# Kernel optimization log

Hardware: AMD Instinct MI355X
Metric: run time of the kernel (lower is better)

## Reference

```python
import jax, jax.numpy as jnp
import numpy as np

EPS = 1e-6          # RMSNorm eps
SINK_EPS = 1e-12    # Sinkhorn denominator eps
N_ITER = 5          # sinkhorn_iters


def setup_inputs() -> dict:
    key = jax.random.key(0)
    ks = jax.random.split(key, 12)
    B, T, H, D = 2, 2048, 4, 2048
    FD = H * D
    W_SCALE = 0.02  # keep gate logits in a non-saturated sigmoid range
    return {
        "x": jax.random.normal(ks[0], (B, T, H, D), jnp.float32),
        "norm_w": jnp.ones((FD,), jnp.float32),
        "w_pre": jax.random.normal(ks[1], (H, FD), jnp.float32) * W_SCALE,
        "w_res": jax.random.normal(ks[2], (H * H, FD), jnp.float32) * W_SCALE,
        "w_post": jax.random.normal(ks[3], (H, FD), jnp.float32) * W_SCALE,
        "alpha_pre": jax.random.uniform(ks[4], (1,), jnp.float32),
        "alpha_res": jax.random.uniform(ks[5], (1,), jnp.float32),
        "alpha_post": jax.random.uniform(ks[6], (1,), jnp.float32),
        "s_pre": jax.random.normal(ks[7], (H,), jnp.float32),
        "s_res": jax.random.normal(ks[8], (H, H), jnp.float32),
        "s_post": jax.random.normal(ks[9], (H,), jnp.float32),
        "w_inner": jax.random.normal(ks[10], (D, D), jnp.float32) * (1.0 / np.sqrt(D)),
    }


def sinkhorn_knopp(logits, n_iter):
    # Doubly-stochastic projection over last two dims.
    m = jnp.exp(logits - jnp.max(logits, axis=(-2, -1), keepdims=True))
    for _ in range(n_iter):
        m = m / (jnp.sum(m, axis=-1, keepdims=True) + SINK_EPS)
        m = m / (jnp.sum(m, axis=-2, keepdims=True) + SINK_EPS)
    return m


def reference(x, norm_w, w_pre, w_res, w_post, alpha_pre, alpha_res, alpha_post,
              s_pre, s_res, s_post, w_inner):
    b, t, h, d = x.shape
    flat = x.reshape(b, t, h * d)
    # RMSNorm over flat dim
    var = jnp.mean(flat * flat, axis=-1, keepdims=True)
    normed = norm_w * flat * jax.lax.rsqrt(var + EPS)
    # Gate projections (Linear, no bias => x @ W.T)
    a_raw = alpha_pre * (normed @ w_pre.T) + s_pre                     # (b,t,h)
    b_raw = (alpha_res * (normed @ w_res.T)).reshape(b, t, h, h) + s_res
    c_raw = alpha_post * (normed @ w_post.T) + s_post                  # (b,t,h)
    a_l = jax.nn.sigmoid(a_raw)
    c_l = 2.0 * jax.nn.sigmoid(c_raw)
    b_l = sinkhorn_knopp(b_raw, N_ITER)
    # split: inner input
    inner_in = jnp.einsum('bth,bthd->btd', a_l, x)
    # inner layer: bias-free linear
    inner_out = inner_in @ w_inner.T
    # combine
    carry = jnp.einsum('bthk,btkd->bthd', b_l, x)
    write = jnp.einsum('bth,btd->bthd', c_l, inner_out)
    return carry + write
```

## Files before the change

kernel.cpp:

```cpp
#include <hip/hip_runtime.h>
#include <hip/hip_bf16.h>

#define FD 8192
#define DD 2048
#define NH 4
#define NT 4096
#define NG 24
#define NGP 32
#define KSPLIT 32
#define KC (FD / KSPLIT)
#define CH 64

typedef __attribute__((ext_vector_type(4))) float f32x4;
typedef __attribute__((ext_vector_type(8))) short short8;

__device__ inline unsigned short f2bf(float f) {
  __hip_bfloat16 h = __float2bfloat16(f);
  unsigned short u; __builtin_memcpy(&u, &h, 2); return u;
}
__device__ inline float bf2f(unsigned short u) {
  __hip_bfloat16 h; __builtin_memcpy(&h, &u, 2); return __bfloat162float(h);
}

__global__ __launch_bounds__(256) void k_prep(
    const float* __restrict__ w_inner,
    const float* __restrict__ w_pre,
    const float* __restrict__ w_res,
    const float* __restrict__ w_post,
    const float* __restrict__ norm_w,
    unsigned short* __restrict__ w_inner_bf,
    unsigned short* __restrict__ wnb)
{
  int stride = gridDim.x * blockDim.x;
  int gid = blockIdx.x * blockDim.x + threadIdx.x;
  for (int i = gid; i < DD * DD; i += stride) w_inner_bf[i] = f2bf(w_inner[i]);
  for (int i = gid; i < NGP * FD; i += stride) {
    int j = i >> 13, k = i & (FD - 1);
    float w = (j < 4) ? w_pre[j * FD + k]
            : (j < 20) ? w_res[(j - 4) * FD + k]
            : (j < 24) ? w_post[(j - 20) * FD + k]
            : 0.0f;
    wnb[i] = f2bf(w * norm_w[k]);
  }
}

__global__ __launch_bounds__(256) void k_gates(
    const float* __restrict__ x, const unsigned short* __restrict__ wnb,
    float* __restrict__ partial ,
    unsigned short* __restrict__ xb )
{
  __shared__ unsigned short xs[128][72];
  const int tb = blockIdx.x;
  const int ks = blockIdx.y;
  const int tid = threadIdx.x;
  const int wave = tid >> 6, lane = tid & 63;
  const int lr = lane & 15, kg = lane >> 4;
  const int t0 = tb * 128;
  const int k0 = ks * KC;
  const int sr = tid >> 4;
  const int sc = (tid & 15) * 4;

  float ssq[8];
#pragma unroll
  for (int i = 0; i < 8; ++i) ssq[i] = 0.f;
  f32x4 acc[2][2] = {};

  for (int ch = 0; ch < KC; ch += CH) {
    __syncthreads();
#pragma unroll
    for (int it = 0; it < 8; ++it) {
      int r = it * 16 + sr;
      size_t goff = (size_t)(t0 + r) * FD + k0 + ch + sc;
      f32x4 v = *(const f32x4*)&x[goff];
      ssq[it] += v.x * v.x + v.y * v.y + v.z * v.z + v.w * v.w;
      ushort4 o;
      o.x = f2bf(v.x); o.y = f2bf(v.y); o.z = f2bf(v.z); o.w = f2bf(v.w);
      *(ushort4*)&xs[r][sc] = o;
      *(ushort4*)&xb[goff] = o;
    }
    __syncthreads();
#pragma unroll
    for (int kk = 0; kk < CH; kk += 32) {
      short8 a[2], b[2];
#pragma unroll
      for (int m = 0; m < 2; ++m)
        a[m] = *(const short8*)&xs[wave * 32 + m * 16 + lr][kk + kg * 8];
#pragma unroll
      for (int n = 0; n < 2; ++n)
        b[n] = *(const short8*)&wnb[(size_t)(n * 16 + lr) * FD + k0 + ch + kk + kg * 8];
#pragma unroll
      for (int m = 0; m < 2; ++m)
#pragma unroll
        for (int n = 0; n < 2; ++n)
          acc[m][n] = __builtin_amdgcn_mfma_f32_16x16x32_bf16(a[m], b[n], acc[m][n], 0, 0, 0);
    }
  }

  float* base = &partial[(size_t)ks * NT * (NG + 1)];
#pragma unroll
  for (int m = 0; m < 2; ++m)
#pragma unroll
    for (int n = 0; n < 2; ++n) {
      int g = n * 16 + lr;
      if (g < NG) {
#pragma unroll
        for (int r = 0; r < 4; ++r) {
          int row = wave * 32 + m * 16 + kg * 4 + r;
          base[(size_t)(t0 + row) * (NG + 1) + g] = acc[m][n][r];
        }
      }
    }
#pragma unroll
  for (int it = 0; it < 8; ++it) {
    float v = ssq[it];
    v += __shfl_xor(v, 1);
    v += __shfl_xor(v, 2);
    v += __shfl_xor(v, 4);
    v += __shfl_xor(v, 8);
    if ((tid & 15) == 0) {
      int row = it * 16 + sr;
      base[(size_t)(t0 + row) * (NG + 1) + NG] = v;
    }
  }
}

__global__ __launch_bounds__(256) void k_scalars(
    const float* __restrict__ partial,
    const float* __restrict__ alpha_pre, const float* __restrict__ alpha_res,
    const float* __restrict__ alpha_post,
    const float* __restrict__ s_pre, const float* __restrict__ s_res,
    const float* __restrict__ s_post,
    float* __restrict__ gates )
{
  int t = blockIdx.x * blockDim.x + threadIdx.x;
  if (t >= NT) return;
  float acc[NG + 1];
#pragma unroll
  for (int j = 0; j <= NG; ++j) acc[j] = 0.f;
  for (int s = 0; s < KSPLIT; ++s) {
    const float* p = &partial[((size_t)s * NT + t) * (NG + 1)];
#pragma unroll
    for (int j = 0; j <= NG; ++j) acc[j] += p[j];
  }
  float rinv = rsqrtf(acc[NG] * (1.0f / FD) + 1e-6f);
  float ap = alpha_pre[0], ar = alpha_res[0], apo = alpha_post[0];

  float out[NG];
#pragma unroll
  for (int h = 0; h < 4; ++h)
    out[h] = 1.f / (1.f + expf(-(ap * rinv * acc[h] + s_pre[h])));
#pragma unroll
  for (int h = 0; h < 4; ++h)
    out[4 + h] = 2.f / (1.f + expf(-(apo * rinv * acc[20 + h] + s_post[h])));

  float m[16]; float mx = -1e30f;
#pragma unroll
  for (int j = 0; j < 16; ++j) {
    float br = ar * rinv * acc[4 + j] + s_res[j];
    m[j] = br; mx = fmaxf(mx, br);
  }
#pragma unroll
  for (int j = 0; j < 16; ++j) m[j] = expf(m[j] - mx);
#pragma unroll
  for (int it = 0; it < 5; ++it) {
#pragma unroll
    for (int h = 0; h < 4; ++h) {
      float rs = m[h*4] + m[h*4+1] + m[h*4+2] + m[h*4+3];
      float inv = 1.f / (rs + 1e-12f);
      m[h*4] *= inv; m[h*4+1] *= inv; m[h*4+2] *= inv; m[h*4+3] *= inv;
    }
#pragma unroll
    for (int k = 0; k < 4; ++k) {
      float cs = m[k] + m[4+k] + m[8+k] + m[12+k];
      float inv = 1.f / (cs + 1e-12f);
      m[k] *= inv; m[4+k] *= inv; m[8+k] *= inv; m[12+k] *= inv;
    }
  }
#pragma unroll
  for (int j = 0; j < 16; ++j) out[8 + j] = m[j];

  float* gt = &gates[(size_t)t * 24];
#pragma unroll
  for (int j = 0; j < NG; ++j) gt[j] = out[j];
}

__global__ __launch_bounds__(256) void k_inner_in(
    const unsigned short* __restrict__ xb, const float* __restrict__ gates,
    unsigned short* __restrict__ inner_in)
{
  int t = blockIdx.x, tid = threadIdx.x;
  const float* g = &gates[(size_t)t * 24];
  float a0 = g[0], a1 = g[1], a2 = g[2], a3 = g[3];
  const unsigned short* xt = &xb[(size_t)t * FD];
  int d = tid * 8;
  short8 h0 = *(const short8*)&xt[0 * DD + d];
  short8 h1 = *(const short8*)&xt[1 * DD + d];
  short8 h2 = *(const short8*)&xt[2 * DD + d];
  short8 h3 = *(const short8*)&xt[3 * DD + d];
  short8 o;
#pragma unroll
  for (int j = 0; j < 8; ++j) {
    float s = a0 * bf2f((unsigned short)h0[j]) + a1 * bf2f((unsigned short)h1[j])
            + a2 * bf2f((unsigned short)h2[j]) + a3 * bf2f((unsigned short)h3[j]);
    o[j] = (short)f2bf(s);
  }
  *(short8*)&inner_in[(size_t)t * DD + d] = o;
}

__global__ __launch_bounds__(256) void k_gemm(
    const unsigned short* __restrict__ A,
    const unsigned short* __restrict__ B,
    unsigned short* __restrict__ C)
{
  __shared__ unsigned short As[128 * 64];
  __shared__ unsigned short Bs[128 * 64];
  const int bid = blockIdx.x;
  const int bm = bid >> 4, bn = bid & 15;
  const int tid = threadIdx.x;
  const int wave = tid >> 6, lane = tid & 63;
  const int wm = wave >> 1, wn_ = wave & 1;
  const int lr = lane & 15, kg = lane >> 4;

  const int srow = tid >> 3;
  const int scol = (tid & 7) * 8;
  const unsigned short* a_src = &A[(size_t)(bm * 128 + srow) * 2048 + scol];
  const unsigned short* b_src = &B[(size_t)(bn * 128 + srow) * 2048 + scol];

  f32x4 acc[4][4] = {};

  for (int kt = 0; kt < 2048; kt += 64) {
    __syncthreads();
#pragma unroll
    for (int it = 0; it < 4; ++it)
      __builtin_amdgcn_global_load_lds(
          (const __attribute__((address_space(1))) void*)(a_src + (size_t)it * 32 * 2048 + kt),
          (__attribute__((address_space(3))) void*)(&As[it * 2048 + tid * 8]), 16, 0, 0);
#pragma unroll
    for (int it = 0; it < 4; ++it)
      __builtin_amdgcn_global_load_lds(
          (const __attribute__((address_space(1))) void*)(b_src + (size_t)it * 32 * 2048 + kt),
          (__attribute__((address_space(3))) void*)(&Bs[it * 2048 + tid * 8]), 16, 0, 0);
    __syncthreads();
#pragma unroll
    for (int kk = 0; kk < 64; kk += 32) {
      short8 a[4], b[4];
#pragma unroll
      for (int m = 0; m < 4; ++m)
        a[m] = *(const short8*)&As[(wm * 64 + m * 16 + lr) * 64 + kk + kg * 8];
#pragma unroll
      for (int n = 0; n < 4; ++n)
        b[n] = *(const short8*)&Bs[(wn_ * 64 + n * 16 + lr) * 64 + kk + kg * 8];
#pragma unroll
      for (int m = 0; m < 4; ++m)
#pragma unroll
        for (int n = 0; n < 4; ++n)
          acc[m][n] = __builtin_amdgcn_mfma_f32_16x16x32_bf16(a[m], b[n], acc[m][n], 0, 0, 0);
    }
  }

  const int row_base = bm * 128 + wm * 64;
  const int col_base = bn * 128 + wn_ * 64;
#pragma unroll
  for (int m = 0; m < 4; ++m)
#pragma unroll
    for (int n = 0; n < 4; ++n) {
      int col = col_base + n * 16 + lr;
#pragma unroll
      for (int r = 0; r < 4; ++r) {
        int row = row_base + m * 16 + kg * 4 + r;
        C[(size_t)row * 2048 + col] = f2bf(acc[m][n][r]);
      }
    }
}

__global__ __launch_bounds__(256) void k_out(
    const unsigned short* __restrict__ xb, const float* __restrict__ gates,
    const unsigned short* __restrict__ inner_out, float* __restrict__ out)
{
  int t = blockIdx.x, tid = threadIdx.x;
  const float* g = &gates[(size_t)t * 24];
  float c[4], bl[16];
#pragma unroll
  for (int h = 0; h < 4; ++h) c[h] = g[4 + h];
#pragma unroll
  for (int j = 0; j < 16; ++j) bl[j] = g[8 + j];
  const unsigned short* xt = &xb[(size_t)t * FD];
  float* ot = &out[(size_t)t * FD];
  int d = tid * 8;
  short8 xh[4];
#pragma unroll
  for (int h = 0; h < 4; ++h) xh[h] = *(const short8*)&xt[h * DD + d];
  short8 iu = *(const short8*)&inner_out[(size_t)t * DD + d];
  float io[8], xf[4][8];
#pragma unroll
  for (int j = 0; j < 8; ++j) io[j] = bf2f((unsigned short)iu[j]);
#pragma unroll
  for (int h = 0; h < 4; ++h)
#pragma unroll
    for (int j = 0; j < 8; ++j) xf[h][j] = bf2f((unsigned short)xh[h][j]);
#pragma unroll
  for (int h = 0; h < 4; ++h) {
    f32x4 o0, o1;
#pragma unroll
    for (int j = 0; j < 4; ++j) {
      o0[j] = c[h] * io[j]     + bl[h*4+0] * xf[0][j]     + bl[h*4+1] * xf[1][j]
                               + bl[h*4+2] * xf[2][j]     + bl[h*4+3] * xf[3][j];
      o1[j] = c[h] * io[j + 4] + bl[h*4+0] * xf[0][j + 4] + bl[h*4+1] * xf[1][j + 4]
                               + bl[h*4+2] * xf[2][j + 4] + bl[h*4+3] * xf[3][j + 4];
    }
    *(f32x4*)&ot[h * DD + d] = o0;
    *(f32x4*)&ot[h * DD + d + 4] = o1;
  }
}

extern "C" void kernel_launch(void* const* d_in, const int* in_sizes, int n_in,
                              void* d_out, int out_size, void* d_ws, size_t ws_size,
                              hipStream_t stream) {
  const float* x          = (const float*)d_in[0];
  const float* norm_w     = (const float*)d_in[1];
  const float* w_pre      = (const float*)d_in[2];
  const float* w_res      = (const float*)d_in[3];
  const float* w_post     = (const float*)d_in[4];
  const float* alpha_pre  = (const float*)d_in[5];
  const float* alpha_res  = (const float*)d_in[6];
  const float* alpha_post = (const float*)d_in[7];
  const float* s_pre      = (const float*)d_in[8];
  const float* s_res      = (const float*)d_in[9];
  const float* s_post     = (const float*)d_in[10];
  const float* w_inner    = (const float*)d_in[11];
  float* out = (float*)d_out;

  char* ws = (char*)d_ws;
  size_t off = 0;
  auto alloc = [&](size_t bytes) -> void* {
    void* p = ws + off;
    off = (off + bytes + 255) & ~(size_t)255;
    return p;
  };
  unsigned short* w_inner_bf = (unsigned short*)alloc((size_t)DD * DD * 2);
  unsigned short* inner_in   = (unsigned short*)alloc((size_t)NT * DD * 2);
  unsigned short* inner_out  = (unsigned short*)alloc((size_t)NT * DD * 2);
  unsigned short* wnb        = (unsigned short*)alloc((size_t)NGP * FD * 2);
  unsigned short* xb         = (unsigned short*)alloc((size_t)NT * FD * 2);
  float* partial = (float*)alloc((size_t)KSPLIT * NT * (NG + 1) * 4);
  float* gates   = (float*)alloc((size_t)NT * 24 * 4);

  k_prep<<<1024, 256, 0, stream>>>(w_inner, w_pre, w_res, w_post, norm_w, w_inner_bf, wnb);
  k_gates<<<dim3(32, 32), 256, 0, stream>>>(x, wnb, partial, xb);
  k_scalars<<<16, 256, 0, stream>>>(partial, alpha_pre, alpha_res, alpha_post,
                                    s_pre, s_res, s_post, gates);
  k_inner_in<<<4096, 256, 0, stream>>>(xb, gates, inner_in);
  k_gemm<<<512, 256, 0, stream>>>(inner_in, w_inner_bf, inner_out);
  k_out<<<4096, 256, 0, stream>>>(xb, gates, inner_out, out);
}
```

Before: 175.1 us.

## Move x bf16 conversion and sum-of-squares into prep; load gate tiles via LDS DMA

The fp32-to-bf16 conversion of x and the per-token sum of squares move into k_prep, one block per token, with extra blocks that convert the weights using vector loads. k_gates then reads the bf16 x through global_load_lds straight into a 64KB LDS tile and runs the MFMA loop without re-staging. The goal is a simpler, more memory-efficient gate GEMM and a smaller partial buffer. In exchange, the bf16 x is now written and then read back by a separate kernel, and the large LDS allocation limits occupancy in k_gates.

```diff
diff --git a/kernel.cpp b/kernel.cpp
--- a/kernel.cpp
+++ b/kernel.cpp
@@ -9,7 +9,6 @@
 #define NGP 32
 #define KSPLIT 32
 #define KC (FD / KSPLIT)
-#define CH 64
 
 typedef __attribute__((ext_vector_type(4))) float f32x4;
 typedef __attribute__((ext_vector_type(8))) short short8;
@@ -23,33 +22,64 @@
 }
 
 __global__ __launch_bounds__(256) void k_prep(
+    const float* __restrict__ x,
     const float* __restrict__ w_inner,
     const float* __restrict__ w_pre,
     const float* __restrict__ w_res,
     const float* __restrict__ w_post,
     const float* __restrict__ norm_w,
+    unsigned short* __restrict__ xb,
+    float* __restrict__ ssq_out,
     unsigned short* __restrict__ w_inner_bf,
     unsigned short* __restrict__ wnb)
 {
-  int stride = gridDim.x * blockDim.x;
-  int gid = blockIdx.x * blockDim.x + threadIdx.x;
-  for (int i = gid; i < DD * DD; i += stride) w_inner_bf[i] = f2bf(w_inner[i]);
-  for (int i = gid; i < NGP * FD; i += stride) {
-    int j = i >> 13, k = i & (FD - 1);
-    float w = (j < 4) ? w_pre[j * FD + k]
-            : (j < 20) ? w_res[(j - 4) * FD + k]
-            : (j < 24) ? w_post[(j - 20) * FD + k]
-            : 0.0f;
-    wnb[i] = f2bf(w * norm_w[k]);
+  const int tid = threadIdx.x;
+  if (blockIdx.x < NT) {
+    const int t = blockIdx.x;
+    const float* xt = &x[(size_t)t * FD];
+    unsigned short* xo = &xb[(size_t)t * FD];
+    float ss = 0.f;
+#pragma unroll
+    for (int it = 0; it < 8; ++it) {
+      int d = (it * 256 + tid) * 4;
+      f32x4 v = *(const f32x4*)&xt[d];
+      ss += v.x * v.x + v.y * v.y + v.z * v.z + v.w * v.w;
+      ushort4 o;
+      o.x = f2bf(v.x); o.y = f2bf(v.y); o.z = f2bf(v.z); o.w = f2bf(v.w);
+      *(ushort4*)&xo[d] = o;
+    }
+#pragma unroll
+    for (int off = 1; off < 64; off <<= 1) ss += __shfl_xor(ss, off);
+    __shared__ float red[4];
+    if ((tid & 63) == 0) red[tid >> 6] = ss;
+    __syncthreads();
+    if (tid == 0) ssq_out[t] = red[0] + red[1] + red[2] + red[3];
+  } else {
+    const int wid = (blockIdx.x - NT) * 256 + tid;
+#pragma unroll
+    for (int it = 0; it < 4; ++it) {
+      int i = wid * 16 + it * 4;
+      f32x4 v = *(const f32x4*)&w_inner[i];
+      ushort4 o;
+      o.x = f2bf(v.x); o.y = f2bf(v.y); o.z = f2bf(v.z); o.w = f2bf(v.w);
+      *(ushort4*)&w_inner_bf[i] = o;
+    }
+    {
+      int j = wid >> 13, k = wid & (FD - 1);
+      float w = (j < 4) ? w_pre[j * FD + k]
+              : (j < 20) ? w_res[(j - 4) * FD + k]
+              : (j < 24) ? w_post[(j - 20) * FD + k]
+              : 0.0f;
+      wnb[wid] = f2bf(w * norm_w[k]);
+    }
   }
 }
 
 __global__ __launch_bounds__(256) void k_gates(
-    const float* __restrict__ x, const unsigned short* __restrict__ wnb,
-    float* __restrict__ partial ,
-    unsigned short* __restrict__ xb )
-{
-  __shared__ unsigned short xs[128][72];
+    const unsigned short* __restrict__ xb, const unsigned short* __restrict__ wnb,
+    float* __restrict__ partial )
+{
+  __shared__ unsigned short As[128 * 256];
   const int tb = blockIdx.x;
   const int ks = blockIdx.y;
   const int tid = threadIdx.x;
@@ -57,46 +87,33 @@
   const int lr = lane & 15, kg = lane >> 4;
   const int t0 = tb * 128;
   const int k0 = ks * KC;
-  const int sr = tid >> 4;
-  const int sc = (tid & 15) * 4;
-
-  float ssq[8];
-#pragma unroll
-  for (int i = 0; i < 8; ++i) ssq[i] = 0.f;
+
+  const unsigned short* src = &xb[(size_t)(t0 + (tid >> 5)) * FD + k0 + (tid & 31) * 8];
+#pragma unroll
+  for (int it = 0; it < 16; ++it)
+    __builtin_amdgcn_global_load_lds(
+        (const __attribute__((address_space(1))) void*)(src + (size_t)(it * 8) * FD),
+        (__attribute__((address_space(3))) void*)(&As[it * 2048 + tid * 8]), 16, 0, 0);
+  __syncthreads();
+
   f32x4 acc[2][2] = {};
-
-  for (int ch = 0; ch < KC; ch += CH) {
-    __syncthreads();
-#pragma unroll
-    for (int it = 0; it < 8; ++it) {
-      int r = it * 16 + sr;
-      size_t goff = (size_t)(t0 + r) * FD + k0 + ch + sc;
-      f32x4 v = *(const f32x4*)&x[goff];
-      ssq[it] += v.x * v.x + v.y * v.y + v.z * v.z + v.w * v.w;
-      ushort4 o;
-      o.x = f2bf(v.x); o.y = f2bf(v.y); o.z = f2bf(v.z); o.w = f2bf(v.w);
-      *(ushort4*)&xs[r][sc] = o;
-      *(ushort4*)&xb[goff] = o;
-    }
-    __syncthreads();
-#pragma unroll
-    for (int kk = 0; kk < CH; kk += 32) {
-      short8 a[2], b[2];
-#pragma unroll
-      for (int m = 0; m < 2; ++m)
-        a[m] = *(const short8*)&xs[wave * 32 + m * 16 + lr][kk + kg * 8];
+#pragma unroll
+  for (int kk = 0; kk < KC; kk += 32) {
+    short8 a[2], b[2];
+#pragma unroll
+    for (int m = 0; m < 2; ++m)
+      a[m] = *(const short8*)&As[(wave * 32 + m * 16 + lr) * 256 + kk + kg * 8];
+#pragma unroll
+    for (int n = 0; n < 2; ++n)
+      b[n] = *(const short8*)&wnb[(size_t)(n * 16 + lr) * FD + k0 + kk + kg * 8];
+#pragma unroll
+    for (int m = 0; m < 2; ++m)
 #pragma unroll
       for (int n = 0; n < 2; ++n)
-        b[n] = *(const short8*)&wnb[(size_t)(n * 16 + lr) * FD + k0 + ch + kk + kg * 8];
-#pragma unroll
-      for (int m = 0; m < 2; ++m)
-#pragma unroll
-        for (int n = 0; n < 2; ++n)
-          acc[m][n] = __builtin_amdgcn_mfma_f32_16x16x32_bf16(a[m], b[n], acc[m][n], 0, 0, 0);
-    }
-  }
-
-  float* base = &partial[(size_t)ks * NT * (NG + 1)];
+        acc[m][n] = __builtin_amdgcn_mfma_f32_16x16x32_bf16(a[m], b[n], acc[m][n], 0, 0, 0);
+  }
+
+  float* base = &partial[(size_t)ks * NT * NG];
 #pragma unroll
   for (int m = 0; m < 2; ++m)
 #pragma unroll
@@ -106,26 +123,14 @@
 #pragma unroll
         for (int r = 0; r < 4; ++r) {
           int row = wave * 32 + m * 16 + kg * 4 + r;
-          base[(size_t)(t0 + row) * (NG + 1) + g] = acc[m][n][r];
+          base[(size_t)(t0 + row) * NG + g] = acc[m][n][r];
         }
       }
     }
-#pragma unroll
-  for (int it = 0; it < 8; ++it) {
-    float v = ssq[it];
-    v += __shfl_xor(v, 1);
-    v += __shfl_xor(v, 2);
-    v += __shfl_xor(v, 4);
-    v += __shfl_xor(v, 8);
-    if ((tid & 15) == 0) {
-      int row = it * 16 + sr;
-      base[(size_t)(t0 + row) * (NG + 1) + NG] = v;
-    }
-  }
 }
 
 __global__ __launch_bounds__(256) void k_scalars(
-    const float* __restrict__ partial,
+    const float* __restrict__ partial, const float* __restrict__ ssq,
     const float* __restrict__ alpha_pre, const float* __restrict__ alpha_res,
     const float* __restrict__ alpha_post,
     const float* __restrict__ s_pre, const float* __restrict__ s_res,
@@ -134,15 +139,15 @@
 {
   int t = blockIdx.x * blockDim.x + threadIdx.x;
   if (t >= NT) return;
-  float acc[NG + 1];
-#pragma unroll
-  for (int j = 0; j <= NG; ++j) acc[j] = 0.f;
+  float acc[NG];
+#pragma unroll
+  for (int j = 0; j < NG; ++j) acc[j] = 0.f;
   for (int s = 0; s < KSPLIT; ++s) {
-    const float* p = &partial[((size_t)s * NT + t) * (NG + 1)];
-#pragma unroll
-    for (int j = 0; j <= NG; ++j) acc[j] += p[j];
-  }
-  float rinv = rsqrtf(acc[NG] * (1.0f / FD) + 1e-6f);
+    const float* p = &partial[((size_t)s * NT + t) * NG];
+#pragma unroll
+    for (int j = 0; j < NG; ++j) acc[j] += p[j];
+  }
+  float rinv = rsqrtf(ssq[t] * (1.0f / FD) + 1e-6f);
   float ap = alpha_pre[0], ar = alpha_res[0], apo = alpha_post[0];
 
   float out[NG];
@@ -342,12 +347,14 @@
   unsigned short* inner_out  = (unsigned short*)alloc((size_t)NT * DD * 2);
   unsigned short* wnb        = (unsigned short*)alloc((size_t)NGP * FD * 2);
   unsigned short* xb         = (unsigned short*)alloc((size_t)NT * FD * 2);
-  float* partial = (float*)alloc((size_t)KSPLIT * NT * (NG + 1) * 4);
+  float* partial = (float*)alloc((size_t)KSPLIT * NT * NG * 4);
   float* gates   = (float*)alloc((size_t)NT * 24 * 4);
-
-  k_prep<<<1024, 256, 0, stream>>>(w_inner, w_pre, w_res, w_post, norm_w, w_inner_bf, wnb);
-  k_gates<<<dim3(32, 32), 256, 0, stream>>>(x, wnb, partial, xb);
-  k_scalars<<<16, 256, 0, stream>>>(partial, alpha_pre, alpha_res, alpha_post,
+  float* ssq     = (float*)alloc((size_t)NT * 4);
+
+  k_prep<<<NT + 1024, 256, 0, stream>>>(x, w_inner, w_pre, w_res, w_post, norm_w,
+                                        xb, ssq, w_inner_bf, wnb);
+  k_gates<<<dim3(32, 32), 256, 0, stream>>>(xb, wnb, partial);
+  k_scalars<<<16, 256, 0, stream>>>(partial, ssq, alpha_pre, alpha_res, alpha_post,
                                     s_pre, s_res, s_post, gates);
   k_inner_in<<<4096, 256, 0, stream>>>(xb, gates, inner_in);
   k_gemm<<<512, 256, 0, stream>>>(inner_in, w_inner_bf, inner_out);
```

Result: slower. 180.0 us (+2.8%).
